# Kernel tuning notes

Hardware: AMD Instinct MI355X
Metric: run time of the kernel (lower is better)

The kernel has to match this reference:

```python
import jax, jax.numpy as jnp
import numpy as np

N = 1_000_000
VOCAB = 50_000
EMBED_DIM = 128
ENCODE_DIM = 128


def _random_preorder_tree(n, seed=0):
    """Generate a random tree whose nodes are numbered in pre-order DFS.
    Returns subtree_end[i] = index of the last node in node i's subtree (inclusive)."""
    rng = np.random.default_rng(seed)
    parent = np.empty(n, dtype=np.int64)
    parent[0] = -1
    stack = [0]
    pops = rng.geometric(0.5, size=n) - 1  # how far up to climb before attaching
    for i in range(1, n):
        npop = min(int(pops[i]), len(stack) - 1)
        for _ in range(npop):
            stack.pop()
        parent[i] = stack[-1]
        stack.append(i)
    end = np.arange(n, dtype=np.int64)
    for i in range(n - 1, 0, -1):
        p = parent[i]
        if end[p] < end[i]:
            end[p] = end[i]
    return end


def setup_inputs() -> dict:
    key = jax.random.key(0)
    k1, k2, k3, k4 = jax.random.split(key, 4)
    tokens = jax.random.randint(k1, (N,), 0, VOCAB, dtype=jnp.int64).astype(jnp.int32)
    subtree_end = jnp.asarray(_random_preorder_tree(N), dtype=jnp.int32)
    embedding_weight = jax.random.normal(k2, (VOCAB, EMBED_DIM), dtype=jnp.float32)
    W = jax.random.normal(k3, (ENCODE_DIM, EMBED_DIM), dtype=jnp.float32) * (1.0 / np.sqrt(EMBED_DIM))
    b = jax.random.normal(k4, (ENCODE_DIM,), dtype=jnp.float32) * 0.01
    return {"tokens": tokens, "subtree_end": subtree_end,
            "embedding_weight": embedding_weight, "W": W, "b": b}


def reference(tokens, subtree_end, embedding_weight, W, b):
    # Per-node contribution: x_i = Linear(Embed(token_i))          [N, encode_dim]
    x = embedding_weight[tokens] @ W.T + b
    # h_i = sum of x over subtree(i). With pre-order DFS numbering, the subtree
    # of i is the contiguous range [i, subtree_end[i]], so use an inclusive
    # prefix sum: h_i = S[end_i] - S[i] + x_i.
    S = jnp.cumsum(x, axis=0)                                      # [N, encode_dim]
    h = S[subtree_end] - S + x                                     # [N, encode_dim]
    # pool = max over all node hidden states (order-independent)
    return jnp.max(h, axis=0)                                      # [encode_dim]
```

## Files before the change

kernel.cpp:

```cpp
#include <hip/hip_runtime.h>
#include <hip/hip_bf16.h>

#define D      128
#define LG     9
#define CHUNK  512

typedef __attribute__((ext_vector_type(8))) short          short8;
typedef __attribute__((ext_vector_type(8))) unsigned short ushort8;
typedef __attribute__((ext_vector_type(4))) float          floatx4;

__device__ inline float b2f(unsigned short u) {
    return __uint_as_float(((unsigned)u) << 16);
}
__device__ inline short f2bf(float f) {
    __hip_bfloat16 h = __float2bfloat16(f);
    unsigned short u;
    __builtin_memcpy(&u, &h, 2);
    return (short)u;
}

__global__ void init_out_kernel(float* out, int out_size) {
    int t = threadIdx.x;
    if (t < out_size) out[t] = -INFINITY;
}

__global__ void local_scan_kernel(const int* __restrict__ tokens,
                                  const float* __restrict__ emb,
                                  unsigned short* __restrict__ S,
                                  float* __restrict__ sumE, int n) {
    __shared__ int toks[CHUNK];
    int c  = blockIdx.x;
    int i0 = c << LG;
    int cnt = min(CHUNK, n - i0);
    for (int t = threadIdx.x; t < cnt; t += 128) toks[t] = tokens[i0 + t];
    __syncthreads();
    int d = threadIdx.x;
    float run = 0.f;
    #pragma unroll 4
    for (int j = 0; j < cnt; ++j) {
        run += emb[(size_t)toks[j] * D + d];
        S[(size_t)(i0 + j) * D + d] = (unsigned short)f2bf(run);
    }
    sumE[(size_t)c * D + d] = run;
}

__global__ void scan_kernel(float* sumE, int C) {
    int d    = blockIdx.x;
    int lane = threadIdx.x;
    float carry = 0.f;
    for (int c0 = 0; c0 < C; c0 += 64) {
        int c = c0 + lane;
        float v = (c < C) ? sumE[(size_t)c * D + d] : 0.f;
        float incl = v;
        #pragma unroll
        for (int off = 1; off < 64; off <<= 1) {
            float t = __shfl_up(incl, off);
            if (lane >= off) incl += t;
        }
        if (c < C) sumE[(size_t)c * D + d] = carry + incl - v;
        carry += __shfl(incl, 63);
    }
}

__device__ inline void atomicMaxF(float* addr, float v) {
    if (v >= 0.f) atomicMax((int*)addr, __float_as_int(v));
    else          atomicMin((unsigned int*)addr, __float_as_uint(v));
}

__global__ __launch_bounds__(256, 2) void max_pass_kernel(
        const int* __restrict__ ends, const unsigned short* __restrict__ S,
        const float* __restrict__ prefE, const float* __restrict__ W,
        const float* __restrict__ bvec, float* __restrict__ out,
        int n, int n_tiles, int tpw) {
    __shared__ float red[4][8][16];
    int lane = threadIdx.x & 63;
    int wid  = threadIdx.x >> 6;
    int c  = lane & 15;
    int kg = lane >> 4;

    short8 Wf[8][4];
    float  bc[8];
    #pragma unroll
    for (int t = 0; t < 8; ++t) {
        const float* wr = W + (size_t)(t * 16 + c) * D + kg * 8;
        bc[t] = bvec[t * 16 + c];
        #pragma unroll
        for (int kk = 0; kk < 4; ++kk) {
            short8 f;
            #pragma unroll
            for (int j = 0; j < 8; ++j) f[j] = f2bf(wr[kk * 32 + j]);
            Wf[t][kk] = f;
        }
    }
    float mx[8];
    #pragma unroll
    for (int t = 0; t < 8; ++t) mx[t] = -INFINITY;

    int gw = blockIdx.x * 4 + wid;
    int t0 = gw * tpw;
    int t1 = min(n_tiles, t0 + tpw);
    for (int tt = t0; tt < t1; ++tt) {
        int base = tt * 16;
        int node = base + c;
        bool vr  = node < n;
        int e  = vr ? ends[node] : 0;
        int p  = node - 1;
        int pc = max(p, 0);
        int ce = e >> LG, cp = pc >> LG;
        bool fast = __all(vr && p >= 0 && ce == cp);
        const ushort8* pe = (const ushort8*)(S + (size_t)e  * D + kg * 8);
        const ushort8* pp = (const ushort8*)(S + (size_t)pc * D + kg * 8);
        short8 A[4];
        if (fast) {
            #pragma unroll
            for (int kk = 0; kk < 4; ++kk) {
                ushort8 se = pe[kk * 4];
                ushort8 sp = pp[kk * 4];
                short8 a;
                #pragma unroll
                for (int j = 0; j < 8; ++j)
                    a[j] = f2bf(b2f(se[j]) - b2f(sp[j]));
                A[kk] = a;
            }
        } else {
            const float* qe = prefE + (size_t)ce * D + kg * 8;
            const float* qp = prefE + (size_t)cp * D + kg * 8;
            float vmask = vr ? 1.f : 0.f;
            float pmask = (p >= 0) ? 1.f : 0.f;
            #pragma unroll
            for (int kk = 0; kk < 4; ++kk) {
                ushort8 se = pe[kk * 4];
                ushort8 sp = pp[kk * 4];
                short8 a;
                #pragma unroll
                for (int j = 0; j < 8; ++j) {
                    float fe = b2f(se[j]) + qe[kk * 32 + j];
                    float fp = b2f(sp[j]) + qp[kk * 32 + j];
                    a[j] = f2bf(vmask * (fe - pmask * fp));
                }
                A[kk] = a;
            }
        }
        floatx4 cnt;
        #pragma unroll
        for (int i = 0; i < 4; ++i) {
            int nd = base + kg * 4 + i;
            cnt[i] = (nd < n) ? (float)(ends[nd] - nd + 1) : 0.f;
        }
        #pragma unroll
        for (int t = 0; t < 8; ++t) {
            floatx4 acc = {0.f, 0.f, 0.f, 0.f};
            #pragma unroll
            for (int kk = 0; kk < 4; ++kk)
                acc = __builtin_amdgcn_mfma_f32_16x16x32_bf16(A[kk], Wf[t][kk], acc, 0, 0, 0);
            #pragma unroll
            for (int i = 0; i < 4; ++i) {
                int nd = base + kg * 4 + i;
                float h = acc[i] + cnt[i] * bc[t];
                if (nd < n) mx[t] = fmaxf(mx[t], h);
            }
        }
    }
    #pragma unroll
    for (int t = 0; t < 8; ++t) {
        float v = mx[t];
        v = fmaxf(v, __shfl_xor(v, 16));
        v = fmaxf(v, __shfl_xor(v, 32));
        mx[t] = v;
    }
    if (kg == 0) {
        #pragma unroll
        for (int t = 0; t < 8; ++t) red[wid][t][c] = mx[t];
    }
    __syncthreads();
    if (threadIdx.x < 128) {
        int t = threadIdx.x >> 4, cc = threadIdx.x & 15;
        float v = fmaxf(fmaxf(red[0][t][cc], red[1][t][cc]),
                        fmaxf(red[2][t][cc], red[3][t][cc]));
        atomicMaxF(&out[t * 16 + cc], v);
    }
}

extern "C" void kernel_launch(void* const* d_in, const int* in_sizes, int n_in,
                              void* d_out, int out_size, void* d_ws, size_t ws_size,
                              hipStream_t stream) {
    const int*   tokens = (const int*)d_in[0];
    const int*   ends   = (const int*)d_in[1];
    const float* emb    = (const float*)d_in[2];
    const float* W      = (const float*)d_in[3];
    const float* bvec   = (const float*)d_in[4];
    float* out = (float*)d_out;
    int n = in_sizes[0];
    int C = (n + CHUNK - 1) >> LG;

    unsigned short* S    = (unsigned short*)d_ws;
    float*          sumE = (float*)(S + (size_t)n * D);

    init_out_kernel<<<1, 128, 0, stream>>>(out, out_size);
    local_scan_kernel<<<C, 128, 0, stream>>>(tokens, emb, S, sumE, n);
    scan_kernel<<<128, 64, 0, stream>>>(sumE, C);

    int n_tiles = (n + 15) / 16;
    int nblocks = 512;
    int tpw = (n_tiles + 2047) / 2048;
    max_pass_kernel<<<nblocks, 256, 0, stream>>>(ends, S, sumE, W, bvec, out,
                                                 n, n_tiles, tpw);
}
```

Before: 292.3 us.

## Stage W fragments in LDS, prefetch ends, raise occupancy and block count

Moves the bf16 W fragments out of per-lane registers (32 short8s) into shared memory, which frees registers so launch bounds can rise to 4 blocks per SM and the grid can double to 1024 blocks. It also prefetches the next tile's subtree ends, computes subtree counts with shuffles instead of extra global loads, vectorizes the prefE loads on the slow path, and raises the local scan unroll to 8. The cost is an LDS read per MFMA operand plus a prologue conversion in every block.

```diff
diff --git a/kernel.cpp b/kernel.cpp
--- a/kernel.cpp
+++ b/kernel.cpp
@@ -36,7 +36,7 @@
     __syncthreads();
     int d = threadIdx.x;
     float run = 0.f;
-    #pragma unroll 4
+    #pragma unroll 8
     for (int j = 0; j < cnt; ++j) {
         run += emb[(size_t)toks[j] * D + d];
         S[(size_t)(i0 + j) * D + d] = (unsigned short)f2bf(run);
@@ -67,31 +67,39 @@
     else          atomicMin((unsigned int*)addr, __float_as_uint(v));
 }
 
-__global__ __launch_bounds__(256, 2) void max_pass_kernel(
+__global__ __launch_bounds__(256, 4) void max_pass_kernel(
         const int* __restrict__ ends, const unsigned short* __restrict__ S,
         const float* __restrict__ prefE, const float* __restrict__ W,
         const float* __restrict__ bvec, float* __restrict__ out,
         int n, int n_tiles, int tpw) {
-    __shared__ float red[4][8][16];
-    int lane = threadIdx.x & 63;
-    int wid  = threadIdx.x >> 6;
+    __shared__ short8 Wlds[2048];
+    __shared__ float  red[4][8][16];
+    int tid = threadIdx.x;
+
+    for (int e = tid; e < 2048; e += 256) {
+        int t  = e >> 8;
+        int kk = (e >> 6) & 3;
+        int cc = (e >> 2) & 15;
+        int kg = e & 3;
+        const float* src = W + (size_t)(t * 16 + cc) * D + kk * 32 + kg * 8;
+        floatx4 f0 = *(const floatx4*)src;
+        floatx4 f1 = *(const floatx4*)(src + 4);
+        short8 w;
+        #pragma unroll
+        for (int j = 0; j < 4; ++j) { w[j] = f2bf(f0[j]); w[j + 4] = f2bf(f1[j]); }
+        Wlds[e] = w;
+    }
+    __syncthreads();
+
+    int lane = tid & 63;
+    int wid  = tid >> 6;
     int c  = lane & 15;
     int kg = lane >> 4;
-
-    short8 Wf[8][4];
-    float  bc[8];
+    int wbase = c * 4 + kg;
+
+    float bc[8];
     #pragma unroll
-    for (int t = 0; t < 8; ++t) {
-        const float* wr = W + (size_t)(t * 16 + c) * D + kg * 8;
-        bc[t] = bvec[t * 16 + c];
-        #pragma unroll
-        for (int kk = 0; kk < 4; ++kk) {
-            short8 f;
-            #pragma unroll
-            for (int j = 0; j < 8; ++j) f[j] = f2bf(wr[kk * 32 + j]);
-            Wf[t][kk] = f;
-        }
-    }
+    for (int t = 0; t < 8; ++t) bc[t] = bvec[t * 16 + c];
     float mx[8];
     #pragma unroll
     for (int t = 0; t < 8; ++t) mx[t] = -INFINITY;
@@ -99,66 +107,82 @@
     int gw = blockIdx.x * 4 + wid;
     int t0 = gw * tpw;
     int t1 = min(n_tiles, t0 + tpw);
-    for (int tt = t0; tt < t1; ++tt) {
-        int base = tt * 16;
-        int node = base + c;
-        bool vr  = node < n;
-        int e  = vr ? ends[node] : 0;
-        int p  = node - 1;
-        int pc = max(p, 0);
-        int ce = e >> LG, cp = pc >> LG;
-        bool fast = __all(vr && p >= 0 && ce == cp);
-        const ushort8* pe = (const ushort8*)(S + (size_t)e  * D + kg * 8);
-        const ushort8* pp = (const ushort8*)(S + (size_t)pc * D + kg * 8);
-        short8 A[4];
-        if (fast) {
-            #pragma unroll
-            for (int kk = 0; kk < 4; ++kk) {
-                ushort8 se = pe[kk * 4];
-                ushort8 sp = pp[kk * 4];
-                short8 a;
-                #pragma unroll
-                for (int j = 0; j < 8; ++j)
-                    a[j] = f2bf(b2f(se[j]) - b2f(sp[j]));
-                A[kk] = a;
+    if (t0 < t1) {
+        int e_cur = ends[min(t0 * 16 + c, n - 1)];
+        for (int tt = t0; tt < t1; ++tt) {
+            int base = tt * 16;
+            int node = base + c;
+            bool vr  = node < n;
+            int e = e_cur;
+            int nidx = (tt + 1 < t1) ? (tt + 1) * 16 + c : node;
+            int e_next = ends[min(nidx, n - 1)];
+            int p  = node - 1;
+            int pc = max(p, 0);
+            int ce = e >> LG, cp = pc >> LG;
+            bool fast = __all(vr && p >= 0 && ce == cp);
+            const ushort8* pe = (const ushort8*)(S + (size_t)e  * D) + kg;
+            const ushort8* pp = (const ushort8*)(S + (size_t)pc * D) + kg;
+            short8 A[4];
+            if (fast) {
+                #pragma unroll
+                for (int kk = 0; kk < 4; ++kk) {
+                    ushort8 se = pe[kk * 4];
+                    ushort8 sp = pp[kk * 4];
+                    short8 a;
+                    #pragma unroll
+                    for (int j = 0; j < 8; ++j)
+                        a[j] = f2bf(b2f(se[j]) - b2f(sp[j]));
+                    A[kk] = a;
+                }
+            } else {
+                const float* qe = prefE + (size_t)ce * D + kg * 8;
+                const float* qp = prefE + (size_t)cp * D + kg * 8;
+                float vmask = vr ? 1.f : 0.f;
+                float pmask = (p >= 0) ? 1.f : 0.f;
+                #pragma unroll
+                for (int kk = 0; kk < 4; ++kk) {
+                    ushort8 se = pe[kk * 4];
+                    ushort8 sp = pp[kk * 4];
+                    floatx4 qe0 = *(const floatx4*)(qe + kk * 32);
+                    floatx4 qe1 = *(const floatx4*)(qe + kk * 32 + 4);
+                    floatx4 qp0 = *(const floatx4*)(qp + kk * 32);
+                    floatx4 qp1 = *(const floatx4*)(qp + kk * 32 + 4);
+                    short8 a;
+                    #pragma unroll
+                    for (int j = 0; j < 4; ++j) {
+                        float fe0 = b2f(se[j])     + qe0[j];
+                        float fp0 = b2f(sp[j])     + qp0[j];
+                        float fe1 = b2f(se[j + 4]) + qe1[j];
+                        float fp1 = b2f(sp[j + 4]) + qp1[j];
+                        a[j]     = f2bf(vmask * (fe0 - pmask * fp0));
+                        a[j + 4] = f2bf(vmask * (fe1 - pmask * fp1));
+                    }
+                    A[kk] = a;
+                }
             }
-        } else {
-            const float* qe = prefE + (size_t)ce * D + kg * 8;
-            const float* qp = prefE + (size_t)cp * D + kg * 8;
-            float vmask = vr ? 1.f : 0.f;
-            float pmask = (p >= 0) ? 1.f : 0.f;
-            #pragma unroll
-            for (int kk = 0; kk < 4; ++kk) {
-                ushort8 se = pe[kk * 4];
-                ushort8 sp = pp[kk * 4];
-                short8 a;
-                #pragma unroll
-                for (int j = 0; j < 8; ++j) {
-                    float fe = b2f(se[j]) + qe[kk * 32 + j];
-                    float fp = b2f(sp[j]) + qp[kk * 32 + j];
-                    a[j] = f2bf(vmask * (fe - pmask * fp));
-                }
-                A[kk] = a;
-            }
-        }
-        floatx4 cnt;
-        #pragma unroll
-        for (int i = 0; i < 4; ++i) {
-            int nd = base + kg * 4 + i;
-            cnt[i] = (nd < n) ? (float)(ends[nd] - nd + 1) : 0.f;
-        }
-        #pragma unroll
-        for (int t = 0; t < 8; ++t) {
-            floatx4 acc = {0.f, 0.f, 0.f, 0.f};
-            #pragma unroll
-            for (int kk = 0; kk < 4; ++kk)
-                acc = __builtin_amdgcn_mfma_f32_16x16x32_bf16(A[kk], Wf[t][kk], acc, 0, 0, 0);
+            floatx4 cnt;
             #pragma unroll
             for (int i = 0; i < 4; ++i) {
                 int nd = base + kg * 4 + i;
-                float h = acc[i] + cnt[i] * bc[t];
-                if (nd < n) mx[t] = fmaxf(mx[t], h);
+                float ee = (float)__shfl(e, kg * 4 + i);
+                cnt[i] = (nd < n) ? (ee - (float)nd + 1.f) : 0.f;
             }
+            #pragma unroll
+            for (int t = 0; t < 8; ++t) {
+                floatx4 acc = {0.f, 0.f, 0.f, 0.f};
+                #pragma unroll
+                for (int kk = 0; kk < 4; ++kk) {
+                    short8 wf = Wlds[t * 256 + kk * 64 + wbase];
+                    acc = __builtin_amdgcn_mfma_f32_16x16x32_bf16(A[kk], wf, acc, 0, 0, 0);
+                }
+                #pragma unroll
+                for (int i = 0; i < 4; ++i) {
+                    int nd = base + kg * 4 + i;
+                    float h = acc[i] + cnt[i] * bc[t];
+                    if (nd < n) mx[t] = fmaxf(mx[t], h);
+                }
+            }
+            e_cur = e_next;
         }
     }
     #pragma unroll
@@ -173,8 +197,8 @@
         for (int t = 0; t < 8; ++t) red[wid][t][c] = mx[t];
     }
     __syncthreads();
-    if (threadIdx.x < 128) {
-        int t = threadIdx.x >> 4, cc = threadIdx.x & 15;
+    if (tid < 128) {
+        int t = tid >> 4, cc = tid & 15;
         float v = fmaxf(fmaxf(red[0][t][cc], red[1][t][cc]),
                         fmaxf(red[2][t][cc], red[3][t][cc]));
         atomicMaxF(&out[t * 16 + cc], v);
@@ -201,8 +225,9 @@
     scan_kernel<<<128, 64, 0, stream>>>(sumE, C);
 
     int n_tiles = (n + 15) / 16;
-    int nblocks = 512;
-    int tpw = (n_tiles + 2047) / 2048;
+    int nblocks = 1024;
+    int gw_cnt  = nblocks * 4;
+    int tpw = (n_tiles + gw_cnt - 1) / gw_cnt;
     max_pass_kernel<<<nblocks, 256, 0, stream>>>(ends, S, sumE, W, bvec, out,
                                                  n, n_tiles, tpw);
 }
```

Result: slower. 382.9 us (+31.0%).
